# Optimization experiments

Measured on AMD Instinct MI355X. Metric: run time of the kernel, lower is better.

## Reference

```python
import jax, jax.numpy as jnp
import numpy as np

B, T, C, H = 4, 2048, 1024, 16
HD = C // H  # head_dim = 64


def setup_inputs() -> dict:
    key = jax.random.key(0)
    ks = jax.random.split(key, 6)
    s_in = 1.0 / np.sqrt(C)
    x = jax.random.normal(ks[0], (B, T, C), dtype=jnp.float32)
    # per-head projection weights, stacked over heads: [H, C, HD]
    Wq = jax.random.uniform(ks[1], (H, C, HD), dtype=jnp.float32, minval=-s_in, maxval=s_in)
    Wk = jax.random.uniform(ks[2], (H, C, HD), dtype=jnp.float32, minval=-s_in, maxval=s_in)
    Wv = jax.random.uniform(ks[3], (H, C, HD), dtype=jnp.float32, minval=-s_in, maxval=s_in)
    # output projection (torch Linear: weight [out,in], bias [out])
    Wp = jax.random.uniform(ks[4], (C, C), dtype=jnp.float32, minval=-s_in, maxval=s_in)
    bp = jax.random.uniform(ks[5], (C,), dtype=jnp.float32, minval=-s_in, maxval=s_in)
    return {"x": x, "Wq": Wq, "Wk": Wk, "Wv": Wv, "Wp": Wp, "bp": bp}


def reference(x, Wq, Wk, Wv, Wp, bp):
    Bx, Tx, Cx = x.shape
    scale = Cx ** 0.5  # NOTE: original scales by embed_dim**0.5, not head_dim**0.5
    q = jnp.einsum('btc,hcd->bhtd', x, Wq)
    k = jnp.einsum('btc,hcd->bhtd', x, Wk)
    v = jnp.einsum('btc,hcd->bhtd', x, Wv)
    # original: einsum('btc,bTc->bTt', q, k) -> logits[b, i, j] = q[b, j] . k[b, i]
    logits = jnp.einsum('bhjd,bhid->bhij', q, k) / scale
    causal = jnp.tril(jnp.ones((Tx, Tx), dtype=bool))  # mask j > i
    logits = jnp.where(causal[None, None], logits, jnp.float32(-jnp.inf))
    weights = jax.nn.softmax(logits, axis=-1)  # [B,H,T,T], the returned attention maps
    # original: einsum('btt,btc->btc', weights, value) -> diagonal of weights scales value
    diag = jnp.diagonal(weights, axis1=-2, axis2=-1)  # [B,H,T]
    attn = diag[..., None] * v  # [B,H,T,HD]
    cat = attn.transpose(0, 2, 1, 3).reshape(Bx, Tx, Cx)  # concat heads on last dim
    out = cat @ Wp.T + bp  # dropout p=0.0 -> identity
    return out, weights
```

## Files before the change

### kernel.cpp

```cpp
#include <hip/hip_runtime.h>


#define NB 4
#define NT 2048
#define NC 1024
#define NH 16
#define NHD 64
#define BH (NB * NH)
typedef unsigned short ushort_t;
#define SLAB ((size_t)NT * (size_t)NT)

typedef __attribute__((ext_vector_type(8))) short short8;
typedef __attribute__((ext_vector_type(4))) float f32x4;

__device__ __forceinline__ ushort_t f2bf(float f) {
    unsigned int x = __float_as_uint(f);
    x += 0x7fffu + ((x >> 16) & 1u);
    return (ushort_t)(x >> 16);
}
__device__ __forceinline__ float bf2f(ushort_t u) {
    return __uint_as_float(((unsigned int)u) << 16);
}

#define GLD_LDS16(g, l) \
    __builtin_amdgcn_global_load_lds( \
        (const __attribute__((address_space(1))) unsigned int*)(g), \
        (__attribute__((address_space(3))) unsigned int*)(l), 16, 0, 0)

__global__ __launch_bounds__(256) void cvt_x(
    const float* __restrict__ x, ushort_t* __restrict__ xbf)
{
    const size_t o = ((size_t)blockIdx.x * 256 + threadIdx.x) * 4;
    float4 u = *(const float4*)(x + o);
    ushort4 v;
    v.x = f2bf(u.x); v.y = f2bf(u.y); v.z = f2bf(u.z); v.w = f2bf(u.w);
    *(ushort4*)(xbf + o) = v;
}

__global__ __launch_bounds__(256) void cvt_w(
    const float* __restrict__ Wq, const float* __restrict__ Wk,
    const float* __restrict__ Wv, ushort_t* __restrict__ Wt)
{
    const int o = blockIdx.x * 256 + threadIdx.x;
    const int sel = o >> 20;
    const int h = (o >> 16) & 15;
    const int idx = o & 65535;
    const int d = idx >> 10, c = idx & 1023;
    const float* W = (sel == 0 ? Wq : (sel == 1 ? Wk : Wv));
    Wt[o] = f2bf(W[(size_t)h * 65536 + (size_t)c * 64 + d]);
}

__global__ __launch_bounds__(256) void cvt_wp(
    const float* __restrict__ Wp, ushort_t* __restrict__ Wpb)
{
    const size_t o = ((size_t)blockIdx.x * 256 + threadIdx.x) * 4;
    float4 u = *(const float4*)(Wp + o);
    ushort4 v;
    v.x = f2bf(u.x); v.y = f2bf(u.y); v.z = f2bf(u.z); v.w = f2bf(u.w);
    *(ushort4*)(Wpb + o) = v;
}

__global__ __launch_bounds__(256) void qkv_gemm2(
    const ushort_t* __restrict__ xbf, const ushort_t* __restrict__ Wt,
    ushort_t* __restrict__ qo, ushort_t* __restrict__ ko, ushort_t* __restrict__ vo)
{
    __shared__ ushort_t smA[128 * 64];
    __shared__ ushort_t smB[128 * 64];
    const int n0 = blockIdx.x * 128;
    const int m0 = blockIdx.y * 128;
    const int tid = threadIdx.x;
    const int wid = tid >> 6, l = tid & 63, lr = l & 15, lg = l >> 4;
    const int wr = wid >> 1, wc = wid & 1;

    const int srow = wid * 32 + (l >> 3);
    const int scol0 = ((l & 7) ^ (srow & 7)) * 8;

    f32x4 acc[4][4];
    #pragma unroll
    for (int i = 0; i < 4; ++i)
        #pragma unroll
        for (int j = 0; j < 4; ++j) acc[i][j] = (f32x4){0.f, 0.f, 0.f, 0.f};

    for (int k0 = 0; k0 < NC; k0 += 64) {
        #pragma unroll
        for (int j = 0; j < 4; ++j) {
            const int row = srow + j * 8;
            GLD_LDS16(xbf + (size_t)(m0 + row) * NC + k0 + scol0,
                      &smA[wid * 2048 + j * 512]);
            GLD_LDS16(Wt + (size_t)(n0 + row) * NC + k0 + scol0,
                      &smB[wid * 2048 + j * 512]);
        }
        __syncthreads();
        short8 a[4][2], b[4][2];
        #pragma unroll
        for (int mi = 0; mi < 4; ++mi) {
            const int rowA = 64 * wr + 16 * mi + lr;
            const int sw = (rowA & 7) * 8;
            a[mi][0] = *(const short8*)&smA[rowA * 64 + ((8 * lg) ^ sw)];
            a[mi][1] = *(const short8*)&smA[rowA * 64 + ((32 + 8 * lg) ^ sw)];
        }
        #pragma unroll
        for (int ni = 0; ni < 4; ++ni) {
            const int rowB = 64 * wc + 16 * ni + lr;
            const int sw = (rowB & 7) * 8;
            b[ni][0] = *(const short8*)&smB[rowB * 64 + ((8 * lg) ^ sw)];
            b[ni][1] = *(const short8*)&smB[rowB * 64 + ((32 + 8 * lg) ^ sw)];
        }
        #pragma unroll
        for (int mi = 0; mi < 4; ++mi)
            #pragma unroll
            for (int ni = 0; ni < 4; ++ni) {
                acc[mi][ni] = __builtin_amdgcn_mfma_f32_16x16x32_bf16(
                    a[mi][0], b[ni][0], acc[mi][ni], 0, 0, 0);
                acc[mi][ni] = __builtin_amdgcn_mfma_f32_16x16x32_bf16(
                    a[mi][1], b[ni][1], acc[mi][ni], 0, 0, 0);
            }
        __syncthreads();
    }
    const int selh = blockIdx.x * 2 + wc;
    const int sel = selh >> 4, h = selh & 15;
    ushort_t* outp = (sel == 0 ? qo : (sel == 1 ? ko : vo));
    #pragma unroll
    for (int mi = 0; mi < 4; ++mi) {
        #pragma unroll
        for (int r = 0; r < 4; ++r) {
            const int m = m0 + 64 * wr + 16 * mi + 4 * lg + r;
            const int bb = m >> 11, tt = m & 2047;
            ushort_t* orow = outp + ((size_t)(bb * NH + h) * NT + tt) * NHD;
            #pragma unroll
            for (int ni = 0; ni < 4; ++ni)
                orow[16 * ni + lr] = f2bf(acc[mi][ni][r]);
        }
    }
}

__global__ __launch_bounds__(256) void scores_mfma(
    const ushort_t* __restrict__ q, const ushort_t* __restrict__ k,
    float* __restrict__ w, float* __restrict__ diag)
{
    __shared__ ushort_t smQ[2][64 * 64];
    const int ib = blockIdx.x, bh = blockIdx.y;
    const int tid = threadIdx.x;
    const int wid = tid >> 6, l = tid & 63, lr = l & 15, lg = l >> 4;
    const int i0 = ib * 64;
    const ushort_t* kb = k + (size_t)bh * (NT * NHD);
    const ushort_t* qb = q + (size_t)bh * (NT * NHD);
    float* wbase = w + (size_t)bh * SLAB;

    short8 af0, af1;
    {
        const ushort_t* kp = kb + (size_t)(i0 + wid * 16 + lr) * NHD + 8 * lg;
        af0 = *(const short8*)kp;
        af1 = *(const short8*)(kp + 32);
    }
    const int gi_base = i0 + wid * 16 + 4 * lg;

    const int srlo = l >> 3;
    const int scol = ((l & 7) ^ srlo) * 8;

    #define STAGEQ(buf, jt)                                                  \
        _Pragma("unroll")                                                    \
        for (int j = 0; j < 2; ++j) {                                        \
            const int row_ = wid * 16 + j * 8 + srlo;                        \
            GLD_LDS16(qb + (size_t)((jt) * 64 + row_) * NHD + scol,          \
                      &smQ[buf][(wid * 16 + j * 8) * 64]);                   \
        }

    float lsum[4] = {0.f, 0.f, 0.f, 0.f};
    STAGEQ(0, 0);
    __syncthreads();
    for (int jt = 0; jt <= ib; ++jt) {
        const int cur = jt & 1;
        if (jt < ib) { STAGEQ(cur ^ 1, jt + 1); }
        #pragma unroll
        for (int nt = 0; nt < 4; ++nt) {
            const int rowB = nt * 16 + lr;
            const int sw = (rowB & 7) * 8;
            const short8 b0 = *(const short8*)&smQ[cur][rowB * 64 + ((8 * lg) ^ sw)];
            const short8 b1 = *(const short8*)&smQ[cur][rowB * 64 + ((32 + 8 * lg) ^ sw)];
            f32x4 acc = {0,0,0,0};
            acc = __builtin_amdgcn_mfma_f32_16x16x32_bf16(af0, b0, acc, 0, 0, 0);
            acc = __builtin_amdgcn_mfma_f32_16x16x32_bf16(af1, b1, acc, 0, 0, 0);
            const int gj = jt * 64 + nt * 16 + lr;
            #pragma unroll
            for (int r = 0; r < 4; ++r) {
                float e = __expf(acc[r] * 0.03125f);
                lsum[r] += (gj <= gi_base + r) ? e : 0.f;
            }
        }
        __syncthreads();
    }
    float linv[4];
    #pragma unroll
    for (int r = 0; r < 4; ++r) {
        float v = lsum[r];
        v += __shfl_xor(v, 1);
        v += __shfl_xor(v, 2);
        v += __shfl_xor(v, 4);
        v += __shfl_xor(v, 8);
        linv[r] = 1.0f / v;
    }
    STAGEQ(0, 0);
    __syncthreads();
    for (int jt = 0; jt <= ib; ++jt) {
        const int cur = jt & 1;
        if (jt < ib) { STAGEQ(cur ^ 1, jt + 1); }
        #pragma unroll
        for (int nt = 0; nt < 4; ++nt) {
            const int rowB = nt * 16 + lr;
            const int sw = (rowB & 7) * 8;
            const short8 b0 = *(const short8*)&smQ[cur][rowB * 64 + ((8 * lg) ^ sw)];
            const short8 b1 = *(const short8*)&smQ[cur][rowB * 64 + ((32 + 8 * lg) ^ sw)];
            f32x4 acc = {0,0,0,0};
            acc = __builtin_amdgcn_mfma_f32_16x16x32_bf16(af0, b0, acc, 0, 0, 0);
            acc = __builtin_amdgcn_mfma_f32_16x16x32_bf16(af1, b1, acc, 0, 0, 0);
            const int gj = jt * 64 + nt * 16 + lr;
            #pragma unroll
            for (int r = 0; r < 4; ++r) {
                const int gi = gi_base + r;
                float e = __expf(acc[r] * 0.03125f) * linv[r];
                e = (gj <= gi) ? e : 0.f;
                __builtin_nontemporal_store(e, &wbase[(size_t)gi * NT + gj]);
                if (gj == gi) diag[(size_t)bh * NT + gi] = e;
            }
        }
        __syncthreads();
    }
    #undef STAGEQ
    const f32x4 z4 = {0.f, 0.f, 0.f, 0.f};
    for (int jt = ib + 1; jt < NT / 64; ++jt) {
        #pragma unroll
        for (int it = 0; it < 4; ++it) {
            const int row = i0 + wid * 16 + it * 4 + lg;
            f32x4* p = (f32x4*)&wbase[(size_t)row * NT + jt * 64 + lr * 4];
            __builtin_nontemporal_store(z4, p);
        }
    }
}

__global__ __launch_bounds__(256) void out_gemm(
    const ushort_t* __restrict__ vs, const float* __restrict__ diag,
    const ushort_t* __restrict__ Wpb, const float* __restrict__ bpv,
    float* __restrict__ out)
{
    __shared__ ushort_t smA[128 * 64];
    __shared__ ushort_t smB[128 * 64];
    const int n0 = blockIdx.x * 128;
    const int m0 = blockIdx.y * 128;
    const int tid = threadIdx.x;
    const int wid = tid >> 6, l = tid & 63, lr = l & 15, lg = l >> 4;
    const int wr = wid >> 1, wc = wid & 1;

    const int srow = wid * 32 + (l >> 3);
    const int scol0 = ((l & 7) ^ (srow & 7)) * 8;

    f32x4 acc[4][4];
    #pragma unroll
    for (int i = 0; i < 4; ++i)
        #pragma unroll
        for (int j = 0; j < 4; ++j) acc[i][j] = (f32x4){0.f, 0.f, 0.f, 0.f};

    for (int k0 = 0; k0 < NC; k0 += 64) {
        const int h = k0 >> 6;
        #pragma unroll
        for (int j = 0; j < 4; ++j) {
            GLD_LDS16(Wpb + (size_t)(n0 + srow + j * 8) * NC + k0 + scol0,
                      &smB[wid * 2048 + j * 512]);
        }
        #pragma unroll
        for (int j = 0; j < 4; ++j) {
            const int row = srow + j * 8;
            const int m = m0 + row, bb = m >> 11, tt = m & 2047;
            const size_t bhT = (size_t)(bb * NH + h) * NT + tt;
            const short8 u = *(const short8*)(vs + bhT * NHD + (l & 7) * 8);
            const float dg = diag[bhT];
            short8 sc;
            #pragma unroll
            for (int e = 0; e < 8; ++e)
                sc[e] = (short)f2bf(bf2f((ushort_t)u[e]) * dg);
            *(short8*)&smA[row * 64 + scol0] = sc;
        }
        __syncthreads();
        short8 a[4][2], b[4][2];
        #pragma unroll
        for (int mi = 0; mi < 4; ++mi) {
            const int rowA = 64 * wr + 16 * mi + lr;
            const int sw = (rowA & 7) * 8;
            a[mi][0] = *(const short8*)&smA[rowA * 64 + ((8 * lg) ^ sw)];
            a[mi][1] = *(const short8*)&smA[rowA * 64 + ((32 + 8 * lg) ^ sw)];
        }
        #pragma unroll
        for (int ni = 0; ni < 4; ++ni) {
            const int rowB = 64 * wc + 16 * ni + lr;
            const int sw = (rowB & 7) * 8;
            b[ni][0] = *(const short8*)&smB[rowB * 64 + ((8 * lg) ^ sw)];
            b[ni][1] = *(const short8*)&smB[rowB * 64 + ((32 + 8 * lg) ^ sw)];
        }
        #pragma unroll
        for (int mi = 0; mi < 4; ++mi)
            #pragma unroll
            for (int ni = 0; ni < 4; ++ni) {
                acc[mi][ni] = __builtin_amdgcn_mfma_f32_16x16x32_bf16(
                    a[mi][0], b[ni][0], acc[mi][ni], 0, 0, 0);
                acc[mi][ni] = __builtin_amdgcn_mfma_f32_16x16x32_bf16(
                    a[mi][1], b[ni][1], acc[mi][ni], 0, 0, 0);
            }
        __syncthreads();
    }
    float bias[4];
    #pragma unroll
    for (int ni = 0; ni < 4; ++ni) bias[ni] = bpv[n0 + 64 * wc + 16 * ni + lr];
    #pragma unroll
    for (int mi = 0; mi < 4; ++mi) {
        #pragma unroll
        for (int r = 0; r < 4; ++r) {
            const int m = m0 + 64 * wr + 16 * mi + 4 * lg + r;
            float* orow = out + (size_t)m * NC + n0 + 64 * wc;
            #pragma unroll
            for (int ni = 0; ni < 4; ++ni)
                __builtin_nontemporal_store(acc[mi][ni][r] + bias[ni],
                                            &orow[16 * ni + lr]);
        }
    }
}

extern "C" void kernel_launch(void* const* d_in, const int* in_sizes, int n_in,
                              void* d_out, int out_size, void* d_ws, size_t ws_size,
                              hipStream_t stream)
{
    const float* x  = (const float*)d_in[0];
    const float* Wq = (const float*)d_in[1];
    const float* Wk = (const float*)d_in[2];
    const float* Wv = (const float*)d_in[3];
    const float* Wp = (const float*)d_in[4];
    const float* bp = (const float*)d_in[5];

    float* out = (float*)d_out;
    float* w = out + (size_t)NB * NT * NC;

    ushort_t* xbf = (ushort_t*)d_ws;
    ushort_t* Wt  = xbf + (size_t)NB * NT * NC;
    ushort_t* qs  = Wt + (size_t)3 * NH * NHD * NC;
    ushort_t* ks  = qs + (size_t)BH * NT * NHD;
    ushort_t* vs  = ks + (size_t)BH * NT * NHD;
    float* diag   = (float*)(vs + (size_t)BH * NT * NHD);
    ushort_t* Wpb = (ushort_t*)(diag + (size_t)BH * NT);

    cvt_x<<<(NB * NT * NC) / 1024, 256, 0, stream>>>(x, xbf);
    cvt_w<<<(3 * NH * NHD * NC) / 256, 256, 0, stream>>>(Wq, Wk, Wv, Wt);
    cvt_wp<<<(NC * NC) / 1024, 256, 0, stream>>>(Wp, Wpb);
    qkv_gemm2<<<dim3(24, 64), 256, 0, stream>>>(xbf, Wt, qs, ks, vs);
    scores_mfma<<<dim3(NT / 64, BH), 256, 0, stream>>>(qs, ks, w, diag);
    out_gemm<<<dim3(8, 64), 256, 0, stream>>>(vs, diag, Wpb, bp, out);
}
```

Before: 454.3 us.

## Fuse conversion kernels, swizzle QKV block order, stage score tiles through LDS

Folds the three fp32-to-bf16 conversion launches into one kernel, which removes launch overhead. It also remaps the QKV GEMM block index with an XCD-aware swizzle so that neighbouring tiles share cache. In the scores kernel, each 64x64 probability tile is first written to a padded LDS buffer and then stored to global as coalesced 16-byte rows, instead of as scattered scalar stores. The cost is an extra LDS buffer and an extra barrier per tile.

Result: faster. 391.7 us (-13.8%).

```diff
diff --git a/kernel.cpp b/kernel.cpp
--- a/kernel.cpp
+++ b/kernel.cpp
@@ -27,37 +27,31 @@
         (const __attribute__((address_space(1))) unsigned int*)(g), \
         (__attribute__((address_space(3))) unsigned int*)(l), 16, 0, 0)
 
-__global__ __launch_bounds__(256) void cvt_x(
-    const float* __restrict__ x, ushort_t* __restrict__ xbf)
-{
-    const size_t o = ((size_t)blockIdx.x * 256 + threadIdx.x) * 4;
-    float4 u = *(const float4*)(x + o);
-    ushort4 v;
-    v.x = f2bf(u.x); v.y = f2bf(u.y); v.z = f2bf(u.z); v.w = f2bf(u.w);
-    *(ushort4*)(xbf + o) = v;
-}
-
-__global__ __launch_bounds__(256) void cvt_w(
-    const float* __restrict__ Wq, const float* __restrict__ Wk,
-    const float* __restrict__ Wv, ushort_t* __restrict__ Wt)
-{
-    const int o = blockIdx.x * 256 + threadIdx.x;
-    const int sel = o >> 20;
-    const int h = (o >> 16) & 15;
-    const int idx = o & 65535;
-    const int d = idx >> 10, c = idx & 1023;
-    const float* W = (sel == 0 ? Wq : (sel == 1 ? Wk : Wv));
-    Wt[o] = f2bf(W[(size_t)h * 65536 + (size_t)c * 64 + d]);
-}
-
-__global__ __launch_bounds__(256) void cvt_wp(
-    const float* __restrict__ Wp, ushort_t* __restrict__ Wpb)
-{
-    const size_t o = ((size_t)blockIdx.x * 256 + threadIdx.x) * 4;
-    float4 u = *(const float4*)(Wp + o);
-    ushort4 v;
-    v.x = f2bf(u.x); v.y = f2bf(u.y); v.z = f2bf(u.z); v.w = f2bf(u.w);
-    *(ushort4*)(Wpb + o) = v;
+__global__ __launch_bounds__(256) void cvt_all(
+    const float* __restrict__ x, const float* __restrict__ Wq,
+    const float* __restrict__ Wk, const float* __restrict__ Wv,
+    const float* __restrict__ Wp,
+    ushort_t* __restrict__ xbf, ushort_t* __restrict__ Wpb,
+    ushort_t* __restrict__ Wt)
+{
+    const int b = blockIdx.x;
+    if (b < 8192 + 1024) {
+        const float* src = (b < 8192) ? x : Wp;
+        ushort_t* dst = (b < 8192) ? xbf : Wpb;
+        const size_t o = ((size_t)(b < 8192 ? b : b - 8192) * 256 + threadIdx.x) * 4;
+        float4 u = *(const float4*)(src + o);
+        ushort4 v;
+        v.x = f2bf(u.x); v.y = f2bf(u.y); v.z = f2bf(u.z); v.w = f2bf(u.w);
+        *(ushort4*)(dst + o) = v;
+    } else {
+        const int o = (b - 9216) * 256 + threadIdx.x;
+        const int sel = o >> 20;
+        const int h = (o >> 16) & 15;
+        const int idx = o & 65535;
+        const int d = idx >> 10, c = idx & 1023;
+        const float* W = (sel == 0 ? Wq : (sel == 1 ? Wk : Wv));
+        Wt[o] = f2bf(W[(size_t)h * 65536 + (size_t)c * 64 + d]);
+    }
 }
 
 __global__ __launch_bounds__(256) void qkv_gemm2(
@@ -66,8 +60,10 @@
 {
     __shared__ ushort_t smA[128 * 64];
     __shared__ ushort_t smB[128 * 64];
-    const int n0 = blockIdx.x * 128;
-    const int m0 = blockIdx.y * 128;
+    const int bid = blockIdx.x;
+    const int swz = (bid & 7) * 192 + (bid >> 3);
+    const int n0 = (swz % 24) * 128;
+    const int m0 = (swz / 24) * 128;
     const int tid = threadIdx.x;
     const int wid = tid >> 6, l = tid & 63, lr = l & 15, lg = l >> 4;
     const int wr = wid >> 1, wc = wid & 1;
@@ -117,7 +113,7 @@
             }
         __syncthreads();
     }
-    const int selh = blockIdx.x * 2 + wc;
+    const int selh = (n0 >> 6) + wc;
     const int sel = selh >> 4, h = selh & 15;
     ushort_t* outp = (sel == 0 ? qo : (sel == 1 ? ko : vo));
     #pragma unroll
@@ -139,6 +135,7 @@
     float* __restrict__ w, float* __restrict__ diag)
 {
     __shared__ ushort_t smQ[2][64 * 64];
+    __shared__ float eT[64][68];
     const int ib = blockIdx.x, bh = blockIdx.y;
     const int tid = threadIdx.x;
     const int wid = tid >> 6, l = tid & 63, lr = l & 15, lg = l >> 4;
@@ -220,9 +217,18 @@
                 const int gi = gi_base + r;
                 float e = __expf(acc[r] * 0.03125f) * linv[r];
                 e = (gj <= gi) ? e : 0.f;
-                __builtin_nontemporal_store(e, &wbase[(size_t)gi * NT + gj]);
+                eT[wid * 16 + 4 * lg + r][nt * 16 + lr] = e;
                 if (gj == gi) diag[(size_t)bh * NT + gi] = e;
             }
+        }
+        __syncthreads();
+        #pragma unroll
+        for (int it = 0; it < 4; ++it) {
+            const int chunk = it * 256 + tid;
+            const int row = chunk >> 4, c4 = chunk & 15;
+            const f32x4 v4 = *(const f32x4*)&eT[row][c4 * 4];
+            __builtin_nontemporal_store(
+                v4, (f32x4*)&wbase[(size_t)(i0 + row) * NT + jt * 64 + c4 * 4]);
         }
         __syncthreads();
     }
@@ -346,10 +352,8 @@
     float* diag   = (float*)(vs + (size_t)BH * NT * NHD);
     ushort_t* Wpb = (ushort_t*)(diag + (size_t)BH * NT);
 
-    cvt_x<<<(NB * NT * NC) / 1024, 256, 0, stream>>>(x, xbf);
-    cvt_w<<<(3 * NH * NHD * NC) / 256, 256, 0, stream>>>(Wq, Wk, Wv, Wt);
-    cvt_wp<<<(NC * NC) / 1024, 256, 0, stream>>>(Wp, Wpb);
-    qkv_gemm2<<<dim3(24, 64), 256, 0, stream>>>(xbf, Wt, qs, ks, vs);
+    cvt_all<<<21504, 256, 0, stream>>>(x, Wq, Wk, Wv, Wp, xbf, Wpb, Wt);
+    qkv_gemm2<<<1536, 256, 0, stream>>>(xbf, Wt, qs, ks, vs);
     scores_mfma<<<dim3(NT / 64, BH), 256, 0, stream>>>(qs, ks, w, diag);
     out_gemm<<<dim3(8, 64), 256, 0, stream>>>(vs, diag, Wpb, bp, out);
 }
```
